# Performance work log

Hardware: AMD Instinct MI355X
Metric: run time of the kernel (lower is better)

Reference implementation:

```python
import jax, jax.numpy as jnp
import numpy as np

FMAP = 160        # feature-map side -> N = FMAP*FMAP anchors
STRIDE = 4.0      # anchor grid stride in pixels
ANCHOR_SIZE = 32.0
NUM_CLASSES = 8
MAX_GT = 50
BATCH = 32


def setup_inputs() -> dict:
    key = jax.random.key(0)
    k0, k1, k2, k3, k4, k5 = jax.random.split(key, 6)
    B, C, H = BATCH, NUM_CLASSES, FMAP
    cls_output = jax.random.normal(k0, (B, C, 1, H, H), jnp.float32)
    reg_output = jax.random.normal(k1, (B, 4, 1, H, H), jnp.float32) * 0.3
    # anchor grid: one ANCHOR_SIZE box per feature-map cell; flatten order
    # matches torch's reshape over (H, W)
    c = (jnp.arange(H, dtype=jnp.float32) + 0.5) * STRIDE
    cy, cx = jnp.meshgrid(c, c, indexing='ij')   # row-major [H, W]
    cx = cx.reshape(-1); cy = cy.reshape(-1)
    half = ANCHOR_SIZE / 2.0
    anchors = jnp.stack([cx - half, cy - half, cx + half, cy + half], axis=1)
    # padded GT boxes, all geometrically valid (x1<x2, y1<y2)
    cxy = jax.random.uniform(k2, (B, MAX_GT, 2), jnp.float32, 64.0, 576.0)
    wh = jax.random.uniform(k3, (B, MAX_GT, 2), jnp.float32, 16.0, 128.0)
    gt_boxes = jnp.concatenate([cxy - wh / 2.0, cxy + wh / 2.0], axis=-1)
    gt_labels = jax.random.randint(k4, (B, MAX_GT), 0, NUM_CLASSES)
    num_boxes = jax.random.randint(k5, (B,), 0, MAX_GT + 1)
    return dict(cls_output=cls_output, reg_output=reg_output, anchors=anchors,
                gt_boxes=gt_boxes, gt_labels=gt_labels, num_boxes=num_boxes)


def _decode_boxes(reg, anchors):
    # inverse of the encoding in the loss: tx=(gt_cx-a_cx)*(4/aw) then (tx+1)/2
    aw = anchors[:, 2] - anchors[:, 0]
    ah = anchors[:, 3] - anchors[:, 1]
    acx = anchors[:, 0] + 0.5 * aw
    acy = anchors[:, 1] + 0.5 * ah
    tx = reg[..., 0] * 2.0 - 1.0
    ty = reg[..., 1] * 2.0 - 1.0
    cx = acx + tx * aw / 4.0
    cy = acy + ty * ah / 4.0
    w = aw * jnp.exp(reg[..., 2])
    h = ah * jnp.exp(reg[..., 3])
    return jnp.stack([cx - w / 2, cy - h / 2, cx + w / 2, cy + h / 2], axis=-1)


def _pairwise_iou(b1, b2):
    # b1 [B,N,4], b2 [B,M,4] -> [B,N,M]
    lt = jnp.maximum(b1[:, :, None, :2], b2[:, None, :, :2])
    rb = jnp.minimum(b1[:, :, None, 2:], b2[:, None, :, 2:])
    wh = jnp.clip(rb - lt, 0.0)
    inter = wh[..., 0] * wh[..., 1]
    a1 = (b1[..., 2] - b1[..., 0]) * (b1[..., 3] - b1[..., 1])
    a2 = (b2[..., 2] - b2[..., 0]) * (b2[..., 3] - b2[..., 1])
    return inter / jnp.maximum(a1[:, :, None] + a2[:, None, :] - inter, 1e-8)


def _smooth_l1(x):
    ax = jnp.abs(x)
    return jnp.where(ax < 1.0, 0.5 * x * x, ax - 0.5)


def _forward(cls_output, reg_output, anchors, gt_boxes, gt_labels, num_boxes):
    B, C = cls_output.shape[0], cls_output.shape[1]
    M = gt_boxes.shape[1]
    cls_i = cls_output.reshape(B, C, -1).transpose(0, 2, 1)   # [B,N,C]
    reg_i = reg_output.reshape(B, 4, -1).transpose(0, 2, 1)   # [B,N,4]
    decoded = _decode_boxes(reg_i, anchors)                    # [B,N,4]
    ious = _pairwise_iou(decoded, gt_boxes)                    # [B,N,M]
    valid = jnp.arange(M)[None, :] < num_boxes[:, None]        # [B,M]
    ious = jnp.where(valid[:, None, :], ious, -1.0)
    max_ious = ious.max(axis=-1)                               # [B,N]
    max_idx = ious.argmax(axis=-1)                             # [B,N]
    has = num_boxes > 0                                        # [B]
    pos = (max_ious >= 0.25) & has[:, None]
    neg = (max_ious < 0.1) & has[:, None]
    # classification
    logp = jax.nn.log_softmax(cls_i, axis=-1)
    tgt = jnp.take_along_axis(gt_labels, max_idx, axis=1)      # [B,N]
    ce_tgt = -jnp.take_along_axis(logp, tgt[..., None], axis=-1)[..., 0]
    ce_bg = -logp[..., 0]
    posf = pos.astype(cls_i.dtype)
    negf = neg.astype(cls_i.dtype)
    npos = posf.sum(-1)
    nneg = negf.sum(-1)
    cls_pos = jnp.where(npos > 0, (ce_tgt * posf).sum(-1) / jnp.maximum(npos, 1.0), 0.0)
    cls_neg = jnp.where(nneg > 0, (ce_bg * negf).sum(-1) / jnp.maximum(nneg, 1.0), 0.0)
    cls_losses = jnp.where(has, cls_pos + cls_neg, ce_bg.mean(-1))
    pg = jnp.take_along_axis(gt_boxes, max_idx[..., None], axis=1)  # [B,N,4]
    aw = anchors[:, 2] - anchors[:, 0]
    ah = anchors[:, 3] - anchors[:, 1]
    acx = anchors[:, 0] + 0.5 * aw
    acy = anchors[:, 1] + 0.5 * ah
    gw = pg[..., 2] - pg[..., 0]
    gh = pg[..., 3] - pg[..., 1]
    gcx = pg[..., 0] + 0.5 * gw
    gcy = pg[..., 1] + 0.5 * gh
    tx = ((gcx - acx) * (4.0 / aw) + 1.0) / 2.0
    ty = ((gcy - acy) * (4.0 / ah) + 1.0) / 2.0
    tw = jnp.log(jnp.maximum(gw, 1e-6) / aw)
    th = jnp.log(jnp.maximum(gh, 1e-6) / ah)
    reg_t = jnp.stack([tx, ty, tw, th], axis=-1)               # [B,N,4]
    sl = _smooth_l1(reg_i - reg_t)
    reg_losses = jnp.where(npos > 0,
                           (sl * posf[..., None]).sum((-1, -2)) / jnp.maximum(npos * 4.0, 1.0),
                           0.0)
    total_pos = npos.sum()
    cls_final = cls_losses.mean()
    reg_final = reg_losses.sum() / jnp.maximum(total_pos, 1.0)
    return cls_final + reg_final, cls_final, reg_final, total_pos


def reference(cls_output, reg_output, anchors, gt_boxes, gt_labels, num_boxes):
    return _forward(cls_output, reg_output, anchors, gt_boxes, gt_labels, num_boxes)
```

## Files before the change

### kernel.cpp

```cpp
#include <hip/hip_runtime.h>

#define FMAP 160
#define NANCH (FMAP * FMAP)
#define NCLS 8
#define MAXGT 50
#define BATCH 32
#define NT 256
#define APT 4
#define ANCH_PER_BLOCK (NT * APT)
#define BLOCKS_PER_B (NANCH / ANCH_PER_BLOCK)

__device__ __forceinline__ float fc(const float4& v, int k) {
    return k == 0 ? v.x : k == 1 ? v.y : k == 2 ? v.z : v.w;
}
__device__ __forceinline__ float sl1(float x) {
    float ax = fabsf(x);
    return ax < 1.f ? 0.5f * x * x : ax - 0.5f;
}

__global__ __launch_bounds__(NT) void detloss_main(
    const float* __restrict__ cls, const float* __restrict__ reg,
    const float* __restrict__ gtb, const int* __restrict__ gtl,
    const int* __restrict__ nb, float* __restrict__ partials)
{
    const int b  = blockIdx.y;
    const int t  = threadIdx.x;
    const int n4 = blockIdx.x * ANCH_PER_BLOCK + 4 * t;

    __shared__ float4 gbox[64];
    __shared__ int    glab[64];
    if (t < MAXGT) {
        gbox[t] = ((const float4*)gtb)[b * MAXGT + t];
        glab[t] = gtl[b * MAXGT + t];
    }
    const int num = nb[b];
    __syncthreads();

    const int vt = blockIdx.x * NT + t;
    const float4* regv = (const float4*)(reg + (size_t)b * 4 * NANCH);
    float4 rx = regv[0 * (NANCH / 4) + vt];
    float4 ry = regv[1 * (NANCH / 4) + vt];
    float4 rw = regv[2 * (NANCH / 4) + vt];
    float4 rh = regv[3 * (NANCH / 4) + vt];
    const float4* clsv = (const float4*)(cls + (size_t)b * NCLS * NANCH);
    float4 L[NCLS];
#pragma unroll
    for (int c = 0; c < NCLS; c++) L[c] = clsv[c * (NANCH / 4) + vt];

    const int row  = n4 / FMAP;
    const int col0 = n4 - row * FMAP;
    const float acx0 = (float)(col0 * 4 + 2);
    const float acy  = (float)(row * 4 + 2);

    float x0[APT], y0[APT], x1[APT], y1[APT], a1[APT];
#pragma unroll
    for (int k = 0; k < APT; k++) {
        float acx = acx0 + 4.f * (float)k;
        float tx = fc(rx, k) * 2.f - 1.f;
        float ty = fc(ry, k) * 2.f - 1.f;
        float cx = acx + tx * 8.f;
        float cy = acy + ty * 8.f;
        float w = 32.f * __expf(fc(rw, k));
        float h = 32.f * __expf(fc(rh, k));
        x0[k] = cx - 0.5f * w; y0[k] = cy - 0.5f * h;
        x1[k] = cx + 0.5f * w; y1[k] = cy + 0.5f * h;
        a1[k] = (x1[k] - x0[k]) * (y1[k] - y0[k]);
    }

    float lse[APT], cebg[APT];
#pragma unroll
    for (int k = 0; k < APT; k++) {
        float s = 0.f;
#pragma unroll
        for (int c = 0; c < NCLS; c++) s += __expf(fc(L[c], k));
        lse[k]  = __logf(s);
        cebg[k] = lse[k] - fc(L[0], k);
    }

    float wx0 = fminf(fminf(x0[0], x0[1]), fminf(x0[2], x0[3]));
    float wy0 = fminf(fminf(y0[0], y0[1]), fminf(y0[2], y0[3]));
    float wx1 = fmaxf(fmaxf(x1[0], x1[1]), fmaxf(x1[2], x1[3]));
    float wy1 = fmaxf(fmaxf(y1[0], y1[1]), fmaxf(y1[2], y1[3]));
#pragma unroll
    for (int o = 1; o < 64; o <<= 1) {
        wx0 = fminf(wx0, __shfl_xor(wx0, o, 64));
        wy0 = fminf(wy0, __shfl_xor(wy0, o, 64));
        wx1 = fmaxf(wx1, __shfl_xor(wx1, o, 64));
        wy1 = fmaxf(wy1, __shfl_xor(wy1, o, 64));
    }

    const int lane = t & 63;
    float4 gme = gbox[lane];
    bool pass = (lane < num) && (gme.x <= wx1) && (gme.z >= wx0)
                            && (gme.y <= wy1) && (gme.w >= wy0);
    unsigned long long mask = __ballot(pass);

    float bi[APT] = {-1.f, -1.f, -1.f, -1.f};
    float bu[APT] = { 1.f,  1.f,  1.f,  1.f};
    int   bidx[APT] = {0, 0, 0, 0};
    int m = mask ? (int)__builtin_ctzll(mask) : 0;
    float4 g = gbox[m];
    unsigned long long rem = mask ? (mask & (mask - 1)) : 0ull;
    while (mask) {
        int mn = rem ? (int)__builtin_ctzll(rem) : 0;
        float4 gn = gbox[mn];
        float ga = (g.z - g.x) * (g.w - g.y);
#pragma unroll
        for (int k = 0; k < APT; k++) {
            float ltx = fmaxf(x0[k], g.x), lty = fmaxf(y0[k], g.y);
            float rbx = fminf(x1[k], g.z), rby = fminf(y1[k], g.w);
            float wx = fmaxf(rbx - ltx, 0.f), wy = fmaxf(rby - lty, 0.f);
            float inter = wx * wy;
            float u = a1[k] + ga - inter;
            bool better = inter * bu[k] > bi[k] * u;
            bi[k]   = better ? inter : bi[k];
            bu[k]   = better ? u     : bu[k];
            bidx[k] = better ? m     : bidx[k];
        }
        m = mn; g = gn; mask = rem; rem = mask ? (mask & (mask - 1)) : 0ull;
    }

    float s_np = 0.f, s_nn = 0.f, s_cp = 0.f, s_cn = 0.f, s_bg = 0.f, s_sl = 0.f;
    const bool has = num > 0;
#pragma unroll
    for (int k = 0; k < APT; k++) {
        s_bg += cebg[k];
        bool pos = has && (bi[k] >= 0.25f * bu[k]);
        bool neg = has && (bi[k] < 0.1f * bu[k]);
        if (neg) { s_nn += 1.f; s_cn += cebg[k]; }
        if (pos) {
            s_np += 1.f;
            int tg = glab[bidx[k]];
            float e0 = (tg & 1) ? fc(L[1], k) : fc(L[0], k);
            float e1 = (tg & 1) ? fc(L[3], k) : fc(L[2], k);
            float e2 = (tg & 1) ? fc(L[5], k) : fc(L[4], k);
            float e3 = (tg & 1) ? fc(L[7], k) : fc(L[6], k);
            float f0 = (tg & 2) ? e1 : e0;
            float f1 = (tg & 2) ? e3 : e2;
            float ltg = (tg & 4) ? f1 : f0;
            s_cp += lse[k] - ltg;
            float4 gp = gbox[bidx[k]];
            float gw = gp.z - gp.x, gh = gp.w - gp.y;
            float gcx = gp.x + 0.5f * gw, gcy = gp.y + 0.5f * gh;
            float acx = acx0 + 4.f * (float)k;
            float txt = ((gcx - acx) * 0.125f + 1.f) * 0.5f;
            float tyt = ((gcy - acy) * 0.125f + 1.f) * 0.5f;
            float twt = __logf(fmaxf(gw, 1e-6f) * 0.03125f);
            float tht = __logf(fmaxf(gh, 1e-6f) * 0.03125f);
            s_sl += sl1(fc(rx, k) - txt) + sl1(fc(ry, k) - tyt)
                  + sl1(fc(rw, k) - twt) + sl1(fc(rh, k) - tht);
        }
    }

#pragma unroll
    for (int o = 32; o > 0; o >>= 1) {
        s_np += __shfl_down(s_np, o, 64);
        s_nn += __shfl_down(s_nn, o, 64);
        s_cp += __shfl_down(s_cp, o, 64);
        s_cn += __shfl_down(s_cn, o, 64);
        s_bg += __shfl_down(s_bg, o, 64);
        s_sl += __shfl_down(s_sl, o, 64);
    }
    __shared__ float red[NT / 64][6];
    const int wid = t >> 6;
    if ((t & 63) == 0) {
        red[wid][0] = s_np; red[wid][1] = s_nn; red[wid][2] = s_cp;
        red[wid][3] = s_cn; red[wid][4] = s_bg; red[wid][5] = s_sl;
    }
    __syncthreads();
    if (t == 0) {
        float* p = partials + (size_t)(b * BLOCKS_PER_B + blockIdx.x) * 6;
#pragma unroll
        for (int j = 0; j < 6; j++)
            p[j] = red[0][j] + red[1][j] + red[2][j] + red[3][j];
    }
}

__global__ __launch_bounds__(64) void detloss_final(
    const float* __restrict__ partials, const int* __restrict__ nb,
    float* __restrict__ out)
{
    const int t = threadIdx.x;
    float np = 0.f, nn = 0.f, cp = 0.f, cn = 0.f, bg = 0.f, sl = 0.f;
    float clsb = 0.f, regb = 0.f;
    if (t < BATCH) {
        for (int i = 0; i < BLOCKS_PER_B; i++) {
            const float* p = partials + (size_t)(t * BLOCKS_PER_B + i) * 6;
            np += p[0]; nn += p[1]; cp += p[2]; cn += p[3]; bg += p[4]; sl += p[5];
        }
        bool has = nb[t] > 0;
        if (has) {
            float a = (np > 0.f) ? cp / fmaxf(np, 1.f) : 0.f;
            float c = (nn > 0.f) ? cn / fmaxf(nn, 1.f) : 0.f;
            clsb = a + c;
        } else {
            clsb = bg / (float)NANCH;
        }
        regb = (np > 0.f) ? sl / fmaxf(np * 4.f, 1.f) : 0.f;
    }
    float tps = np;
#pragma unroll
    for (int o = 32; o > 0; o >>= 1) {
        clsb += __shfl_down(clsb, o, 64);
        regb += __shfl_down(regb, o, 64);
        tps  += __shfl_down(tps,  o, 64);
    }
    if (t == 0) {
        float clsf = clsb / (float)BATCH;
        float regf = regb / fmaxf(tps, 1.f);
        out[0] = clsf + regf;
        out[1] = clsf;
        out[2] = regf;
        out[3] = tps;
    }
}

extern "C" void kernel_launch(void* const* d_in, const int* in_sizes, int n_in,
                              void* d_out, int out_size, void* d_ws, size_t ws_size,
                              hipStream_t stream) {
    const float* cls = (const float*)d_in[0];
    const float* reg = (const float*)d_in[1];
    const float* gtb = (const float*)d_in[3];
    const int*   gtl = (const int*)d_in[4];
    const int*   nb  = (const int*)d_in[5];
    float* out      = (float*)d_out;
    float* partials = (float*)d_ws;

    dim3 grid(BLOCKS_PER_B, BATCH);
    detloss_main<<<grid, NT, 0, stream>>>(cls, reg, gtb, gtl, nb, partials);
    detloss_final<<<1, 64, 0, stream>>>(partials, nb, out);
}
```

Baseline: 19.57 us.

## Use single-wave blocks, y-band GT culling, packed counters and parallel final reduction

Shrinks the main kernel to one 64-thread wave per block. This removes the shared-memory cross-wave reduction and the barriers, and moves the GT staging after the global loads. GT culling now tests only a y-band built from the block's rows and the maximum decoded box height, and GT areas are precomputed in shared memory. Positive and negative counts are packed into one float, so each block emits five partials instead of six. The final kernel spreads the partial reduction over 256 threads instead of 32 serial loops. The y-only culling may let more GT boxes through than the previous x/y window, and dropping the barrier relies on single-wave LDS ordering.

```diff
diff --git a/kernel.cpp b/kernel.cpp
--- a/kernel.cpp
+++ b/kernel.cpp
@@ -5,10 +5,11 @@
 #define NCLS 8
 #define MAXGT 50
 #define BATCH 32
-#define NT 256
+#define NT 64
 #define APT 4
 #define ANCH_PER_BLOCK (NT * APT)
 #define BLOCKS_PER_B (NANCH / ANCH_PER_BLOCK)
+#define PSTRIDE 8
 
 __device__ __forceinline__ float fc(const float4& v, int k) {
     return k == 0 ? v.x : k == 1 ? v.y : k == 2 ? v.z : v.w;
@@ -25,18 +26,10 @@
 {
     const int b  = blockIdx.y;
     const int t  = threadIdx.x;
-    const int n4 = blockIdx.x * ANCH_PER_BLOCK + 4 * t;
-
-    __shared__ float4 gbox[64];
-    __shared__ int    glab[64];
-    if (t < MAXGT) {
-        gbox[t] = ((const float4*)gtb)[b * MAXGT + t];
-        glab[t] = gtl[b * MAXGT + t];
-    }
-    const int num = nb[b];
-    __syncthreads();
-
+    const int nA = blockIdx.x * ANCH_PER_BLOCK;
+    const int n4 = nA + 4 * t;
     const int vt = blockIdx.x * NT + t;
+
     const float4* regv = (const float4*)(reg + (size_t)b * 4 * NANCH);
     float4 rx = regv[0 * (NANCH / 4) + vt];
     float4 ry = regv[1 * (NANCH / 4) + vt];
@@ -47,12 +40,24 @@
 #pragma unroll
     for (int c = 0; c < NCLS; c++) L[c] = clsv[c * (NANCH / 4) + vt];
 
+    __shared__ float4 gbox[64];
+    __shared__ float  garea[64];
+    __shared__ int    glab[64];
+    if (t < MAXGT) {
+        float4 g = ((const float4*)gtb)[b * MAXGT + t];
+        gbox[t]  = g;
+        garea[t] = (g.z - g.x) * (g.w - g.y);
+        glab[t]  = gtl[b * MAXGT + t];
+    }
+    const int num = nb[b];
+
     const int row  = n4 / FMAP;
     const int col0 = n4 - row * FMAP;
     const float acx0 = (float)(col0 * 4 + 2);
     const float acy  = (float)(row * 4 + 2);
 
     float x0[APT], y0[APT], x1[APT], y1[APT], a1[APT];
+    float hmax;
 #pragma unroll
     for (int k = 0; k < APT; k++) {
         float acx = acx0 + 4.f * (float)k;
@@ -64,7 +69,8 @@
         float h = 32.f * __expf(fc(rh, k));
         x0[k] = cx - 0.5f * w; y0[k] = cy - 0.5f * h;
         x1[k] = cx + 0.5f * w; y1[k] = cy + 0.5f * h;
-        a1[k] = (x1[k] - x0[k]) * (y1[k] - y0[k]);
+        a1[k] = w * h;
+        hmax = (k == 0) ? h : fmaxf(hmax, h);
     }
 
     float lse[APT], cebg[APT];
@@ -77,34 +83,23 @@
         cebg[k] = lse[k] - fc(L[0], k);
     }
 
-    float wx0 = fminf(fminf(x0[0], x0[1]), fminf(x0[2], x0[3]));
-    float wy0 = fminf(fminf(y0[0], y0[1]), fminf(y0[2], y0[3]));
-    float wx1 = fmaxf(fmaxf(x1[0], x1[1]), fmaxf(x1[2], x1[3]));
-    float wy1 = fmaxf(fmaxf(y1[0], y1[1]), fmaxf(y1[2], y1[3]));
-#pragma unroll
-    for (int o = 1; o < 64; o <<= 1) {
-        wx0 = fminf(wx0, __shfl_xor(wx0, o, 64));
-        wy0 = fminf(wy0, __shfl_xor(wy0, o, 64));
-        wx1 = fmaxf(wx1, __shfl_xor(wx1, o, 64));
-        wy1 = fmaxf(wy1, __shfl_xor(wy1, o, 64));
-    }
-
-    const int lane = t & 63;
-    float4 gme = gbox[lane];
-    bool pass = (lane < num) && (gme.x <= wx1) && (gme.z >= wx0)
-                            && (gme.y <= wy1) && (gme.w >= wy0);
+#pragma unroll
+    for (int o = 1; o < 64; o <<= 1) hmax = fmaxf(hmax, __shfl_xor(hmax, o, 64));
+    const int rA = nA / FMAP, rB = (nA + ANCH_PER_BLOCK - 1) / FMAP;
+    const float ylo = (float)(rA * 4 + 2) - 8.f - 0.5f * hmax;
+    const float yhi = (float)(rB * 4 + 2) + 8.f + 0.5f * hmax;
+    float gy0 = gbox[t].y, gy1 = gbox[t].w;
+    bool pass = (t < num) && (gy0 <= yhi) && (gy1 >= ylo);
     unsigned long long mask = __ballot(pass);
 
     float bi[APT] = {-1.f, -1.f, -1.f, -1.f};
     float bu[APT] = { 1.f,  1.f,  1.f,  1.f};
     int   bidx[APT] = {0, 0, 0, 0};
-    int m = mask ? (int)__builtin_ctzll(mask) : 0;
-    float4 g = gbox[m];
-    unsigned long long rem = mask ? (mask & (mask - 1)) : 0ull;
     while (mask) {
-        int mn = rem ? (int)__builtin_ctzll(rem) : 0;
-        float4 gn = gbox[mn];
-        float ga = (g.z - g.x) * (g.w - g.y);
+        int m = (int)__builtin_ctzll(mask);
+        mask &= mask - 1;
+        float4 g  = gbox[m];
+        float  ga = garea[m];
 #pragma unroll
         for (int k = 0; k < APT; k++) {
             float ltx = fmaxf(x0[k], g.x), lty = fmaxf(y0[k], g.y);
@@ -117,19 +112,18 @@
             bu[k]   = better ? u     : bu[k];
             bidx[k] = better ? m     : bidx[k];
         }
-        m = mn; g = gn; mask = rem; rem = mask ? (mask & (mask - 1)) : 0ull;
-    }
-
-    float s_np = 0.f, s_nn = 0.f, s_cp = 0.f, s_cn = 0.f, s_bg = 0.f, s_sl = 0.f;
+    }
+
+    float s_pk = 0.f, s_cp = 0.f, s_cn = 0.f, s_bg = 0.f, s_sl = 0.f;
     const bool has = num > 0;
 #pragma unroll
     for (int k = 0; k < APT; k++) {
         s_bg += cebg[k];
         bool pos = has && (bi[k] >= 0.25f * bu[k]);
         bool neg = has && (bi[k] < 0.1f * bu[k]);
-        if (neg) { s_nn += 1.f; s_cn += cebg[k]; }
+        s_pk += pos ? 1.f : (neg ? 4096.f : 0.f);
+        s_cn += neg ? cebg[k] : 0.f;
         if (pos) {
-            s_np += 1.f;
             int tg = glab[bidx[k]];
             float e0 = (tg & 1) ? fc(L[1], k) : fc(L[0], k);
             float e1 = (tg & 1) ? fc(L[3], k) : fc(L[2], k);
@@ -154,64 +148,79 @@
 
 #pragma unroll
     for (int o = 32; o > 0; o >>= 1) {
-        s_np += __shfl_down(s_np, o, 64);
-        s_nn += __shfl_down(s_nn, o, 64);
+        s_pk += __shfl_down(s_pk, o, 64);
         s_cp += __shfl_down(s_cp, o, 64);
         s_cn += __shfl_down(s_cn, o, 64);
         s_bg += __shfl_down(s_bg, o, 64);
         s_sl += __shfl_down(s_sl, o, 64);
     }
-    __shared__ float red[NT / 64][6];
-    const int wid = t >> 6;
-    if ((t & 63) == 0) {
-        red[wid][0] = s_np; red[wid][1] = s_nn; red[wid][2] = s_cp;
-        red[wid][3] = s_cn; red[wid][4] = s_bg; red[wid][5] = s_sl;
-    }
-    __syncthreads();
     if (t == 0) {
-        float* p = partials + (size_t)(b * BLOCKS_PER_B + blockIdx.x) * 6;
-#pragma unroll
-        for (int j = 0; j < 6; j++)
-            p[j] = red[0][j] + red[1][j] + red[2][j] + red[3][j];
-    }
-}
-
-__global__ __launch_bounds__(64) void detloss_final(
+        float* p = partials + (size_t)(b * BLOCKS_PER_B + blockIdx.x) * PSTRIDE;
+        float4 v = make_float4(s_pk, s_cp, s_cn, s_bg);
+        *(float4*)p = v;
+        p[4] = s_sl;
+    }
+}
+
+__global__ __launch_bounds__(256) void detloss_final(
     const float* __restrict__ partials, const int* __restrict__ nb,
     float* __restrict__ out)
 {
     const int t = threadIdx.x;
+    const int img = t >> 3, sub = t & 7;
     float np = 0.f, nn = 0.f, cp = 0.f, cn = 0.f, bg = 0.f, sl = 0.f;
-    float clsb = 0.f, regb = 0.f;
-    if (t < BATCH) {
-        for (int i = 0; i < BLOCKS_PER_B; i++) {
-            const float* p = partials + (size_t)(t * BLOCKS_PER_B + i) * 6;
-            np += p[0]; nn += p[1]; cp += p[2]; cn += p[3]; bg += p[4]; sl += p[5];
-        }
-        bool has = nb[t] > 0;
-        if (has) {
+    for (int j = 0; j < 13; ++j) {
+        int blk = sub + (j << 3);
+        if (blk < BLOCKS_PER_B) {
+            const float* p = partials + (size_t)(img * BLOCKS_PER_B + blk) * PSTRIDE;
+            float pk  = p[0];
+            float nnv = floorf(pk * (1.f / 4096.f));
+            np += pk - 4096.f * nnv;
+            nn += nnv;
+            cp += p[1]; cn += p[2]; bg += p[3]; sl += p[4];
+        }
+    }
+#pragma unroll
+    for (int o = 4; o > 0; o >>= 1) {
+        np += __shfl_down(np, o, 8);
+        nn += __shfl_down(nn, o, 8);
+        cp += __shfl_down(cp, o, 8);
+        cn += __shfl_down(cn, o, 8);
+        bg += __shfl_down(bg, o, 8);
+        sl += __shfl_down(sl, o, 8);
+    }
+    __shared__ float acc[32][4];
+    if (sub == 0) {
+        bool hasb = nb[img] > 0;
+        float clsb;
+        if (hasb) {
             float a = (np > 0.f) ? cp / fmaxf(np, 1.f) : 0.f;
             float c = (nn > 0.f) ? cn / fmaxf(nn, 1.f) : 0.f;
             clsb = a + c;
         } else {
             clsb = bg / (float)NANCH;
         }
-        regb = (np > 0.f) ? sl / fmaxf(np * 4.f, 1.f) : 0.f;
-    }
-    float tps = np;
-#pragma unroll
-    for (int o = 32; o > 0; o >>= 1) {
-        clsb += __shfl_down(clsb, o, 64);
-        regb += __shfl_down(regb, o, 64);
-        tps  += __shfl_down(tps,  o, 64);
-    }
-    if (t == 0) {
-        float clsf = clsb / (float)BATCH;
-        float regf = regb / fmaxf(tps, 1.f);
-        out[0] = clsf + regf;
-        out[1] = clsf;
-        out[2] = regf;
-        out[3] = tps;
+        float regb = (np > 0.f) ? sl / fmaxf(np * 4.f, 1.f) : 0.f;
+        acc[img][0] = clsb; acc[img][1] = regb; acc[img][2] = np;
+    }
+    __syncthreads();
+    if (t < 64) {
+        float c = 0.f, r = 0.f, tp = 0.f;
+        if (t < 32) { c = acc[t][0]; r = acc[t][1]; tp = acc[t][2]; }
+#pragma unroll
+        for (int o = 32; o > 0; o >>= 1) {
+            c  += __shfl_down(c,  o, 64);
+            r  += __shfl_down(r,  o, 64);
+            tp += __shfl_down(tp, o, 64);
+        }
+        if (t == 0) {
+            float clsf = c / (float)BATCH;
+            float regf = r / fmaxf(tp, 1.f);
+            out[0] = clsf + regf;
+            out[1] = clsf;
+            out[2] = regf;
+            out[3] = tp;
+        }
     }
 }
 
@@ -228,5 +237,5 @@
 
     dim3 grid(BLOCKS_PER_B, BATCH);
     detloss_main<<<grid, NT, 0, stream>>>(cls, reg, gtb, gtl, nb, partials);
-    detloss_final<<<1, 64, 0, stream>>>(partials, nb, out);
-}
+    detloss_final<<<1, 256, 0, stream>>>(partials, nb, out);
+}
```

New measurement: 22.74 us. +16.2%, slower.
